# Kernel optimization log

Measured on AMD Instinct MI355X. Metric: run time of the kernel, lower is better.

## Reference

```python
import jax, jax.numpy as jnp
import numpy as np

NEG_SLOPE = 0.2  # PyG GATConv default negative_slope
BN_EPS = 1e-5


def gat_layer(x, src, dst, W, b, a_src, a_dst, heads, out_ch, concat):
    # x: [N, Fin]; W: [Fin, heads*out_ch]; a_src/a_dst: [heads, out_ch]
    N = x.shape[0]
    h = (x @ W).reshape(N, heads, out_ch)
    s = (h * a_src).sum(-1)            # [N, H]
    d = (h * a_dst).sum(-1)            # [N, H]
    e = jax.nn.leaky_relu(s[src] + d[dst], NEG_SLOPE)   # [E, H]
    # segment softmax over incoming edges of each destination node
    m = jax.ops.segment_max(e, dst, num_segments=N)
    ex = jnp.exp(e - m[dst])
    denom = jax.ops.segment_sum(ex, dst, num_segments=N)
    alpha = ex / (denom[dst] + 1e-16)                   # [E, H]
    out = jax.ops.segment_sum(alpha[:, :, None] * h[src], dst, num_segments=N)  # [N,H,C]
    out = out.reshape(N, heads * out_ch) if concat else out.mean(axis=1)
    return out + b


def batchnorm(x, gamma, beta):
    mu = x.mean(axis=0)
    var = x.var(axis=0)
    return gamma * (x - mu) * jax.lax.rsqrt(var + BN_EPS) + beta


def setup_inputs() -> dict:
    key = jax.random.key(0)
    ks = jax.random.split(key, 24)
    N, E, Fin, Hd, heads, C = 50000, 800000, 128, 64, 4, 2
    wdim = Hd * heads  # 256
    inp = {
        'x': jax.random.normal(ks[0], (N, Fin), jnp.float32),
        'edge_index': jax.random.randint(ks[1], (2, E), 0, N, jnp.int64),
    }
    def glorot(k, shape):
        fan = shape[0] + shape[-1]
        return jax.random.normal(k, shape, jnp.float32) * np.sqrt(2.0 / fan)
    # layer 0: Fin -> heads x Hd (concat)
    inp['W0'] = glorot(ks[2], (Fin, wdim)); inp['b0'] = jnp.zeros((wdim,), jnp.float32)
    inp['asrc0'] = glorot(ks[3], (heads, Hd)); inp['adst0'] = glorot(ks[4], (heads, Hd))
    inp['g0'] = jnp.ones((wdim,), jnp.float32); inp['be0'] = jnp.zeros((wdim,), jnp.float32)
    # layer 1: wdim -> heads x Hd (concat)
    inp['W1'] = glorot(ks[5], (wdim, wdim)); inp['b1'] = jnp.zeros((wdim,), jnp.float32)
    inp['asrc1'] = glorot(ks[6], (heads, Hd)); inp['adst1'] = glorot(ks[7], (heads, Hd))
    inp['g1'] = jnp.ones((wdim,), jnp.float32); inp['be1'] = jnp.zeros((wdim,), jnp.float32)
    # layer 2: wdim -> 1 head x Hd (no concat)
    inp['W2'] = glorot(ks[8], (wdim, Hd)); inp['b2'] = jnp.zeros((Hd,), jnp.float32)
    inp['asrc2'] = glorot(ks[9], (1, Hd)); inp['adst2'] = glorot(ks[10], (1, Hd))
    inp['g2'] = jnp.ones((Hd,), jnp.float32); inp['be2'] = jnp.zeros((Hd,), jnp.float32)
    # classifier: Linear(2*Hd, Hd) -> ReLU -> Linear(Hd, C)
    inp['Wc1'] = glorot(ks[11], (2 * Hd, Hd)); inp['bc1'] = jnp.zeros((Hd,), jnp.float32)
    inp['Wc2'] = glorot(ks[12], (Hd, C)); inp['bc2'] = jnp.zeros((C,), jnp.float32)
    return inp


def reference(x, edge_index, W0, b0, asrc0, adst0, g0, be0,
              W1, b1, asrc1, adst1, g1, be1,
              W2, b2, asrc2, adst2, g2, be2,
              Wc1, bc1, Wc2, bc2):
    N = x.shape[0]
    # add self-loops (PyG GATConv default)
    loops = jnp.arange(N, dtype=edge_index.dtype)
    src = jnp.concatenate([edge_index[0], loops])
    dst = jnp.concatenate([edge_index[1], loops])
    heads, Hd = asrc0.shape[0], asrc0.shape[1]

    h = gat_layer(x, src, dst, W0, b0, asrc0, adst0, heads, Hd, True)
    h = jax.nn.relu(batchnorm(h, g0, be0))
    h = gat_layer(h, src, dst, W1, b1, asrc1, adst1, heads, Hd, True)
    h = jax.nn.relu(batchnorm(h, g1, be1))
    h = gat_layer(h, src, dst, W2, b2, asrc2, adst2, 1, Hd, False)
    h = jax.nn.relu(batchnorm(h, g2, be2))

    pooled = jnp.concatenate([h.mean(axis=0, keepdims=True),
                              h.max(axis=0, keepdims=True)], axis=1)  # [1, 2*Hd]
    z = jax.nn.relu(pooled @ Wc1 + bc1)
    return z @ Wc2 + bc2  # [1, num_classes]
```

## Files before the change

kernel.cpp:

```cpp
#include <hip/hip_runtime.h>


typedef unsigned int uint;
typedef unsigned short ushort;

#define NEG_SLOPE 0.2f
#define BN_EPS 1e-5f
#define NB_RED 256

__device__ __forceinline__ float bf2f(uint u) { return __uint_as_float(u << 16); }
__device__ __forceinline__ ushort f2bf(float f) {
    uint u = __float_as_uint(f);
    u += 0x7fff + ((u >> 16) & 1);
    return (ushort)(u >> 16);
}
__device__ __forceinline__ float lrelu(float x) { return x > 0.f ? x : NEG_SLOPE * x; }


__global__ void hist_kernel(const int* __restrict__ ei, int* __restrict__ deg, int E) {
    int e = blockIdx.x * blockDim.x + threadIdx.x;
    if (e < E) atomicAdd(&deg[ei[E + e]], 1);
}

__global__ void scan_part(const int* __restrict__ deg, int* __restrict__ offsets,
                          int* __restrict__ bsum, int N) {
    __shared__ int sh[256];
    int t = threadIdx.x;
    int base = blockIdx.x * 1024 + t * 4;
    int v0 = (base + 0 < N) ? deg[base + 0] : 0;
    int v1 = (base + 1 < N) ? deg[base + 1] : 0;
    int v2 = (base + 2 < N) ? deg[base + 2] : 0;
    int v3 = (base + 3 < N) ? deg[base + 3] : 0;
    int s = v0 + v1 + v2 + v3;
    sh[t] = s;
    __syncthreads();
    for (int off = 1; off < 256; off <<= 1) {
        int y = (t >= off) ? sh[t - off] : 0;
        __syncthreads();
        sh[t] += y;
        __syncthreads();
    }
    int p = sh[t] - s;
    if (base + 0 < N) offsets[base + 0] = p;
    p += v0;
    if (base + 1 < N) offsets[base + 1] = p;
    p += v1;
    if (base + 2 < N) offsets[base + 2] = p;
    p += v2;
    if (base + 3 < N) offsets[base + 3] = p;
    if (t == 255) bsum[blockIdx.x] = sh[255];
}

__global__ void scan_top(const int* __restrict__ bsum, int* __restrict__ bexcl,
                         int nb, int* __restrict__ offsets, int N) {
    if (threadIdx.x == 0) {
        int run = 0;
        for (int b = 0; b < nb; ++b) { bexcl[b] = run; run += bsum[b]; }
        offsets[N] = run;
    }
}

__global__ void scan_add(int* __restrict__ offsets, int* __restrict__ cursor,
                         const int* __restrict__ bexcl, int N) {
    int add = bexcl[blockIdx.x];
    int base = blockIdx.x * 1024 + threadIdx.x * 4;
#pragma unroll
    for (int k = 0; k < 4; ++k) {
        int i = base + k;
        if (i < N) { int v = offsets[i] + add; offsets[i] = v; cursor[i] = v; }
    }
}

__global__ void scatter_kernel(const int* __restrict__ ei, int* __restrict__ cursor,
                               int* __restrict__ srcs, int E) {
    int e = blockIdx.x * blockDim.x + threadIdx.x;
    if (e < E) {
        int s = ei[e];
        int d = ei[E + e];
        int p = atomicAdd(&cursor[d], 1);
        srcs[p] = s;
    }
}


__global__ void cvt_x_kernel(const float* __restrict__ x, ushort* __restrict__ xb,
                             int total_real, int total_pad) {
    int i = blockIdx.x * blockDim.x + threadIdx.x;
    if (i < total_pad) xb[i] = (i < total_real) ? f2bf(x[i]) : (ushort)0;
}

__global__ void transpose_all_kernel(const float* __restrict__ W0, ushort* __restrict__ w0t,
                                     const float* __restrict__ W1, ushort* __restrict__ w1t,
                                     const float* __restrict__ W2, ushort* __restrict__ w2t) {
    int i = blockIdx.x * blockDim.x + threadIdx.x;
    if (i < 32768) {
        int n = i / 128, k = i - n * 128;
        w0t[i] = f2bf(W0[(size_t)k * 256 + n]);
    } else if (i < 32768 + 65536) {
        int j = i - 32768;
        int n = j / 256, k = j - n * 256;
        w1t[j] = f2bf(W1[(size_t)k * 256 + n]);
    } else if (i < 32768 + 65536 + 16384) {
        int j = i - 32768 - 65536;
        int n = j / 256, k = j - n * 256;
        w2t[j] = f2bf(W2[(size_t)k * 64 + n]);
    }
}


typedef __attribute__((ext_vector_type(8))) short bf16x8;
typedef __attribute__((ext_vector_type(4))) float floatx4;

template <int BN, int H>
__launch_bounds__(256)
__global__ void mfma_gemm_bt(const ushort* __restrict__ A, const ushort* __restrict__ Bt,
                             ushort* __restrict__ C, const float* __restrict__ asrc,
                             const float* __restrict__ adst, float* __restrict__ sv,
                             float* __restrict__ dv, int K, int Nn) {
    constexpr int WCOLS = (BN == 128) ? 2 : 1;
    constexpr int WROWS = 4 / WCOLS;
    constexpr int MT = 128 / (WROWS * 16);
    constexpr int NT = BN / (WCOLS * 16);
    constexpr int BCALLS = (BN * 32 * 2) / 4096;

    __shared__ ushort As[128 * 32];
    __shared__ ushort Bs[BN * 32];

    int t = threadIdx.x;
    int w = t >> 6, l = t & 63;
    int row0 = blockIdx.x * 128;
    int col0 = blockIdx.y * BN;
    int wr = (w / WCOLS) * (MT * 16);
    int wc = (w % WCOLS) * (NT * 16);

    floatx4 acc[MT][NT];
#pragma unroll
    for (int mi = 0; mi < MT; ++mi)
#pragma unroll
        for (int ni = 0; ni < NT; ++ni)
#pragma unroll
            for (int r = 0; r < 4; ++r) acc[mi][ni][r] = 0.f;

    int mrow = l & 15;
    int kc = (l >> 4) * 8;

    for (int kt = 0; kt < K; kt += 32) {
#pragma unroll
        for (int c = 0; c < 2; ++c) {
            int idx = c * 256 + t;
            const ushort* gp = A + (size_t)(row0 + (idx >> 2)) * K + kt + (idx & 3) * 8;
            __builtin_amdgcn_global_load_lds(
                (const __attribute__((address_space(1))) void*)gp,
                (__attribute__((address_space(3))) void*)(As + (idx & ~63) * 8),
                16, 0, 0);
        }
#pragma unroll
        for (int c = 0; c < BCALLS; ++c) {
            int idx = c * 256 + t;
            const ushort* gp = Bt + (size_t)(col0 + (idx >> 2)) * K + kt + (idx & 3) * 8;
            __builtin_amdgcn_global_load_lds(
                (const __attribute__((address_space(1))) void*)gp,
                (__attribute__((address_space(3))) void*)(Bs + (idx & ~63) * 8),
                16, 0, 0);
        }
        __syncthreads();

        bf16x8 af[MT], bfr[NT];
#pragma unroll
        for (int mi = 0; mi < MT; ++mi)
            af[mi] = *(const bf16x8*)&As[(wr + mi * 16 + mrow) * 32 + kc];
#pragma unroll
        for (int ni = 0; ni < NT; ++ni)
            bfr[ni] = *(const bf16x8*)&Bs[(wc + ni * 16 + mrow) * 32 + kc];
#pragma unroll
        for (int mi = 0; mi < MT; ++mi)
#pragma unroll
            for (int ni = 0; ni < NT; ++ni)
                acc[mi][ni] = __builtin_amdgcn_mfma_f32_16x16x32_bf16(
                    af[mi], bfr[ni], acc[mi][ni], 0, 0, 0);
        __syncthreads();
    }

#pragma unroll
    for (int mi = 0; mi < MT; ++mi) {
        int rbase = row0 + wr + mi * 16 + (l >> 4) * 4;
#pragma unroll
        for (int ni = 0; ni < NT; ++ni) {
            int col = col0 + wc + ni * 16 + (l & 15);
#pragma unroll
            for (int r = 0; r < 4; ++r)
                C[(size_t)(rbase + r) * Nn + col] = f2bf(acc[mi][ni][r]);
        }
    }

    float av[NT], bv[NT];
#pragma unroll
    for (int ni = 0; ni < NT; ++ni) {
        int ch = col0 + wc + ni * 16 + (l & 15);
        av[ni] = asrc[ch];
        bv[ni] = adst[ch];
    }
    int gh = (col0 + wc) >> 6;
#pragma unroll
    for (int mi = 0; mi < MT; ++mi) {
#pragma unroll
        for (int r = 0; r < 4; ++r) {
            float s = 0.f, d = 0.f;
#pragma unroll
            for (int ni = 0; ni < NT; ++ni) {
                float hv = acc[mi][ni][r];
                s += hv * av[ni];
                d += hv * bv[ni];
            }
#pragma unroll
            for (int m = 8; m >= 1; m >>= 1) {
                s += __shfl_xor(s, m);
                d += __shfl_xor(d, m);
            }
            if ((l & 15) == 0) {
                int row = row0 + wr + mi * 16 + (l >> 4) * 4 + r;
                sv[row * H + gh] = s;
                dv[row * H + gh] = d;
            }
        }
    }
}


__launch_bounds__(128)
__global__ void agg4_kernel(const ushort* __restrict__ hb, const float* __restrict__ sv,
                            const float* __restrict__ dv, const int* __restrict__ offsets,
                            const int* __restrict__ srcs, const float* __restrict__ bias,
                            ushort* __restrict__ zb, int N) {
    int i = blockIdx.x;
    int t = threadIdx.x, g = t >> 5;
    int beg = offsets[i], end = offsets[i + 1];

    float d_i = dv[i * 4 + g];
    float wself = __expf(fminf(lrelu(sv[i * 4 + g] + d_i), 60.f));

    uint p = *(const uint*)&hb[(size_t)i * 256 + 2 * t];
    float ax = wself * bf2f(p & 0xffffu);
    float ay = wself * bf2f(p >> 16);
    float den = wself;

    int j = beg;
    int srcn_next = (j < end) ? srcs[j] : 0;
    for (; j < end;) {
        int srcn = srcn_next;
        float sval = sv[srcn * 4 + g];
        uint q = *(const uint*)&hb[(size_t)srcn * 256 + 2 * t];
        ++j;
        if (j < end) srcn_next = srcs[j];
        float wgt = __expf(fminf(lrelu(sval + d_i), 60.f));
        ax += wgt * bf2f(q & 0xffffu);
        ay += wgt * bf2f(q >> 16);
        den += wgt;
    }
    float rden = 1.f / (den + 1e-16f);
    ax = ax * rden + bias[2 * t];
    ay = ay * rden + bias[2 * t + 1];
    *(uint*)&zb[(size_t)i * 256 + 2 * t] = (uint)f2bf(ax) | ((uint)f2bf(ay) << 16);
}

__launch_bounds__(64)
__global__ void agg1_kernel(const ushort* __restrict__ hb, const float* __restrict__ sv,
                            const float* __restrict__ dv, const int* __restrict__ offsets,
                            const int* __restrict__ srcs, const float* __restrict__ bias,
                            ushort* __restrict__ zb, int N) {
    int i = blockIdx.x;
    int lane = threadIdx.x;
    int beg = offsets[i], end = offsets[i + 1];

    float d_i = dv[i];
    float wself = __expf(fminf(lrelu(sv[i] + d_i), 60.f));
    float acc = wself * bf2f(hb[(size_t)i * 64 + lane]);
    float den = wself;

    int j = beg;
    int srcn_next = (j < end) ? srcs[j] : 0;
    for (; j < end;) {
        int srcn = srcn_next;
        float sval = sv[srcn];
        float hv = bf2f(hb[(size_t)srcn * 64 + lane]);
        ++j;
        if (j < end) srcn_next = srcs[j];
        float wgt = __expf(fminf(lrelu(sval + d_i), 60.f));
        acc += wgt * hv;
        den += wgt;
    }
    zb[(size_t)i * 64 + lane] = f2bf(acc / (den + 1e-16f) + bias[lane]);
}


template <int F>
__launch_bounds__(256)
__global__ void bn_stats_kernel(const ushort* __restrict__ x, float* __restrict__ ps,
                                float* __restrict__ pq, int N) {
    constexpr int OCT = F / 8;
    __shared__ float lds_s[F], lds_q[F];
    int t = threadIdx.x;
    if (t < F) { lds_s[t] = 0.f; lds_q[t] = 0.f; }
    __syncthreads();

    float s[8] = {}, q[8] = {};
    int total8 = N * F / 8;
    for (int idx = blockIdx.x * 256 + t; idx < total8; idx += NB_RED * 256) {
        uint4 v = ((const uint4*)x)[idx];
        uint pr[4] = {v.x, v.y, v.z, v.w};
#pragma unroll
        for (int k = 0; k < 4; ++k) {
            float a = bf2f(pr[k] & 0xffffu);
            float b = bf2f(pr[k] >> 16);
            s[2 * k] += a;     q[2 * k] += a * a;
            s[2 * k + 1] += b; q[2 * k + 1] += b * b;
        }
    }
    int co = t % OCT;
#pragma unroll
    for (int j = 0; j < 8; ++j) {
        atomicAdd(&lds_s[co * 8 + j], s[j]);
        atomicAdd(&lds_q[co * 8 + j], q[j]);
    }
    __syncthreads();
    if (t < F) {
        ps[blockIdx.x * F + t] = lds_s[t];
        pq[blockIdx.x * F + t] = lds_q[t];
    }
}

__global__ void bn_final_kernel(const float* __restrict__ ps, const float* __restrict__ pq,
                                const float* __restrict__ g, const float* __restrict__ be,
                                float* __restrict__ scale, float* __restrict__ shift,
                                int N, int F) {
    int t = threadIdx.x;
    if (t < F) {
        float s = 0.f, q = 0.f;
        for (int b = 0; b < NB_RED; ++b) { s += ps[b * F + t]; q += pq[b * F + t]; }
        float mean = s / (float)N;
        float var = q / (float)N - mean * mean;
        float sc = g[t] * rsqrtf(var + BN_EPS);
        scale[t] = sc;
        shift[t] = be[t] - sc * mean;
    }
}

__global__ void bn_apply_kernel(uint* __restrict__ x, const float* __restrict__ scale,
                                const float* __restrict__ shift, int totalPairs, int Fmask) {
    int i = blockIdx.x * blockDim.x + threadIdx.x;
    if (i < totalPairs) {
        uint p = x[i];
        int c0 = (2 * i) & Fmask;
        float v0 = fmaxf(bf2f(p & 0xffffu) * scale[c0] + shift[c0], 0.f);
        float v1 = fmaxf(bf2f(p >> 16) * scale[c0 + 1] + shift[c0 + 1], 0.f);
        x[i] = (uint)f2bf(v0) | ((uint)f2bf(v1) << 16);
    }
}


__launch_bounds__(256)
__global__ void pool_kernel(const ushort* __restrict__ y, const float* __restrict__ scale,
                            const float* __restrict__ shift, float* __restrict__ psum,
                            float* __restrict__ pmax, int N) {
    constexpr int F = 64, OCT = 8;
    __shared__ float lds_s[F];
    __shared__ uint lds_m[F];
    int t = threadIdx.x;
    if (t < F) { lds_s[t] = 0.f; lds_m[t] = 0u; }
    __syncthreads();

    int co = t % OCT;
    float sc[8], sh[8];
#pragma unroll
    for (int j = 0; j < 8; ++j) { sc[j] = scale[co * 8 + j]; sh[j] = shift[co * 8 + j]; }

    float s[8] = {}, m[8] = {};
    int total8 = N * F / 8;
    for (int idx = blockIdx.x * 256 + t; idx < total8; idx += NB_RED * 256) {
        uint4 v = ((const uint4*)y)[idx];
        uint pr[4] = {v.x, v.y, v.z, v.w};
#pragma unroll
        for (int k = 0; k < 4; ++k) {
            float a = fmaxf(bf2f(pr[k] & 0xffffu) * sc[2 * k] + sh[2 * k], 0.f);
            float b = fmaxf(bf2f(pr[k] >> 16) * sc[2 * k + 1] + sh[2 * k + 1], 0.f);
            s[2 * k] += a;     m[2 * k] = fmaxf(m[2 * k], a);
            s[2 * k + 1] += b; m[2 * k + 1] = fmaxf(m[2 * k + 1], b);
        }
    }
#pragma unroll
    for (int j = 0; j < 8; ++j) {
        atomicAdd(&lds_s[co * 8 + j], s[j]);
        atomicMax(&lds_m[co * 8 + j], __float_as_uint(m[j]));
    }
    __syncthreads();
    if (t < F) {
        psum[blockIdx.x * F + t] = lds_s[t];
        pmax[blockIdx.x * F + t] = __uint_as_float(lds_m[t]);
    }
}

__global__ void classify_kernel(const float* __restrict__ psum, const float* __restrict__ pmax,
                                const float* __restrict__ Wc1, const float* __restrict__ bc1,
                                const float* __restrict__ Wc2, const float* __restrict__ bc2,
                                float* __restrict__ out, int N) {
    __shared__ float pooled[128];
    __shared__ float z[64];
    int t = threadIdx.x;
    if (t < 64) {
        float s = 0.f;
        for (int b = 0; b < NB_RED; ++b) s += psum[b * 64 + t];
        pooled[t] = s / (float)N;
    } else {
        int c = t - 64;
        float m = 0.f;
        for (int b = 0; b < NB_RED; ++b) m = fmaxf(m, pmax[b * 64 + c]);
        pooled[t] = m;
    }
    __syncthreads();
    if (t < 64) {
        float a = bc1[t];
        for (int k = 0; k < 128; ++k) a += pooled[k] * Wc1[k * 64 + t];
        z[t] = a > 0.f ? a : 0.f;
    }
    __syncthreads();
    if (t < 2) {
        float a = bc2[t];
        for (int j = 0; j < 64; ++j) a += z[j] * Wc2[j * 2 + t];
        out[t] = a;
    }
}


extern "C" void kernel_launch(void* const* d_in, const int* in_sizes, int n_in,
                              void* d_out, int out_size, void* d_ws, size_t ws_size,
                              hipStream_t stream) {
    const float* x   = (const float*)d_in[0];
    const int*   ei  = (const int*)d_in[1];
    const float* W0  = (const float*)d_in[2];  const float* b0  = (const float*)d_in[3];
    const float* as0 = (const float*)d_in[4];  const float* ad0 = (const float*)d_in[5];
    const float* g0  = (const float*)d_in[6];  const float* be0 = (const float*)d_in[7];
    const float* W1  = (const float*)d_in[8];  const float* b1  = (const float*)d_in[9];
    const float* as1 = (const float*)d_in[10]; const float* ad1 = (const float*)d_in[11];
    const float* g1  = (const float*)d_in[12]; const float* be1 = (const float*)d_in[13];
    const float* W2  = (const float*)d_in[14]; const float* b2  = (const float*)d_in[15];
    const float* as2 = (const float*)d_in[16]; const float* ad2 = (const float*)d_in[17];
    const float* g2  = (const float*)d_in[18]; const float* be2 = (const float*)d_in[19];
    const float* Wc1 = (const float*)d_in[20]; const float* bc1 = (const float*)d_in[21];
    const float* Wc2 = (const float*)d_in[22]; const float* bc2 = (const float*)d_in[23];
    float* out = (float*)d_out;

    const int N = in_sizes[0] / 128;
    const int E = in_sizes[1] / 2;
    const int Mpad = ((N + 127) / 128) * 128;
    const int NB_SCAN = (N + 1023) / 1024;

    char* ws = (char*)d_ws;
    size_t o = 0;
    auto alloc = [&](size_t bytes) -> void* {
        void* p = ws + o;
        o = (o + bytes + 255) & ~(size_t)255;
        return p;
    };
    int*    deg     = (int*)alloc((size_t)N * 4);
    int*    offsets = (int*)alloc((size_t)(N + 1) * 4);
    int*    cursor  = (int*)alloc((size_t)N * 4);
    int*    srcs    = (int*)alloc((size_t)E * 4);
    int*    bsum    = (int*)alloc((size_t)NB_SCAN * 4);
    int*    bexcl   = (int*)alloc((size_t)NB_SCAN * 4);
    ushort* xb      = (ushort*)alloc((size_t)Mpad * 128 * 2);
    ushort* w0t     = (ushort*)alloc((size_t)256 * 128 * 2);
    ushort* w1t     = (ushort*)alloc((size_t)256 * 256 * 2);
    ushort* w2t     = (ushort*)alloc((size_t)64 * 256 * 2);
    ushort* hb      = (ushort*)alloc((size_t)Mpad * 256 * 2);
    ushort* zb      = (ushort*)alloc((size_t)Mpad * 256 * 2);
    float*  sv      = (float*)alloc((size_t)Mpad * 4 * 4);
    float*  dv      = (float*)alloc((size_t)Mpad * 4 * 4);
    float*  ps      = (float*)alloc((size_t)NB_RED * 256 * 4);
    float*  pq      = (float*)alloc((size_t)NB_RED * 256 * 4);
    float*  scale   = (float*)alloc(256 * 4);
    float*  shift   = (float*)alloc(256 * 4);
    float*  psum    = (float*)alloc((size_t)NB_RED * 64 * 4);
    float*  pmax    = (float*)alloc((size_t)NB_RED * 64 * 4);

    hipMemsetAsync(deg, 0, (size_t)N * 4, stream);
    int eb = (E + 255) / 256;
    hist_kernel<<<eb, 256, 0, stream>>>(ei, deg, E);
    scan_part<<<NB_SCAN, 256, 0, stream>>>(deg, offsets, bsum, N);
    scan_top<<<1, 64, 0, stream>>>(bsum, bexcl, NB_SCAN, offsets, N);
    scan_add<<<NB_SCAN, 256, 0, stream>>>(offsets, cursor, bexcl, N);
    scatter_kernel<<<eb, 256, 0, stream>>>(ei, cursor, srcs, E);

    cvt_x_kernel<<<(Mpad * 128 + 255) / 256, 256, 0, stream>>>(x, xb, N * 128, Mpad * 128);
    transpose_all_kernel<<<(32768 + 65536 + 16384 + 255) / 256, 256, 0, stream>>>(
        W0, w0t, W1, w1t, W2, w2t);

    {
        dim3 gg(Mpad / 128, 2);
        mfma_gemm_bt<128, 4><<<gg, 256, 0, stream>>>(xb, w0t, hb, as0, ad0, sv, dv, 128, 256);
        agg4_kernel<<<N, 128, 0, stream>>>(hb, sv, dv, offsets, srcs, b0, zb, N);
        bn_stats_kernel<256><<<NB_RED, 256, 0, stream>>>(zb, ps, pq, N);
        bn_final_kernel<<<1, 256, 0, stream>>>(ps, pq, g0, be0, scale, shift, N, 256);
        bn_apply_kernel<<<(N * 128 + 255) / 256, 256, 0, stream>>>((uint*)zb, scale, shift,
                                                                   N * 128, 255);
    }
    {
        dim3 gg(Mpad / 128, 2);
        mfma_gemm_bt<128, 4><<<gg, 256, 0, stream>>>(zb, w1t, hb, as1, ad1, sv, dv, 256, 256);
        agg4_kernel<<<N, 128, 0, stream>>>(hb, sv, dv, offsets, srcs, b1, zb, N);
        bn_stats_kernel<256><<<NB_RED, 256, 0, stream>>>(zb, ps, pq, N);
        bn_final_kernel<<<1, 256, 0, stream>>>(ps, pq, g1, be1, scale, shift, N, 256);
        bn_apply_kernel<<<(N * 128 + 255) / 256, 256, 0, stream>>>((uint*)zb, scale, shift,
                                                                   N * 128, 255);
    }
    {
        dim3 gg(Mpad / 128, 1);
        mfma_gemm_bt<64, 1><<<gg, 256, 0, stream>>>(zb, w2t, hb, as2, ad2, sv, dv, 256, 64);
        agg1_kernel<<<N, 64, 0, stream>>>(hb, sv, dv, offsets, srcs, b2, zb, N);
        bn_stats_kernel<64><<<NB_RED, 256, 0, stream>>>(zb, ps, pq, N);
        bn_final_kernel<<<1, 64, 0, stream>>>(ps, pq, g2, be2, scale, shift, N, 64);
    }

    pool_kernel<<<NB_RED, 256, 0, stream>>>(zb, scale, shift, psum, pmax, N);
    classify_kernel<<<1, 128, 0, stream>>>(psum, pmax, Wc1, bc1, Wc2, bc2, out, N);
}
```

Before: 686.6 us.

## Split neighbor aggregation across edge groups with vector loads, fuse prep kernels

The aggregation kernels now process four incoming edges in parallel, one per thread group. Each thread loads a wider vector of features (16 bytes per lane in agg4, 8 bytes in agg1), and the partial sums are reduced through LDS or shuffles before the self-loop term and normalization are applied. This aims to expose more memory-level parallelism in the latency-bound gather over irregular neighbor lists. Separately, the x conversion, weight transposes and degree histogram are merged into one launch to cut launch overhead. In exchange, agg4 adds an LDS reduction and a barrier, and the summation order changes.

```diff
diff --git a/kernel.cpp b/kernel.cpp
--- a/kernel.cpp
+++ b/kernel.cpp
@@ -17,10 +17,39 @@
 __device__ __forceinline__ float lrelu(float x) { return x > 0.f ? x : NEG_SLOPE * x; }
 
 
-__global__ void hist_kernel(const int* __restrict__ ei, int* __restrict__ deg, int E) {
-    int e = blockIdx.x * blockDim.x + threadIdx.x;
-    if (e < E) atomicAdd(&deg[ei[E + e]], 1);
-}
+__global__ void prep_kernel(const float* __restrict__ x, ushort* __restrict__ xb,
+                            int total_real, int total_pad,
+                            const float* __restrict__ W0, ushort* __restrict__ w0t,
+                            const float* __restrict__ W1, ushort* __restrict__ w1t,
+                            const float* __restrict__ W2, ushort* __restrict__ w2t,
+                            const int* __restrict__ ei, int* __restrict__ deg, int E) {
+    int i = blockIdx.x * blockDim.x + threadIdx.x;
+    if (i < total_pad) {
+        xb[i] = (i < total_real) ? f2bf(x[i]) : (ushort)0;
+        return;
+    }
+    int j = i - total_pad;
+    if (j < 32768) {
+        int n = j / 128, k = j - n * 128;
+        w0t[j] = f2bf(W0[(size_t)k * 256 + n]);
+        return;
+    }
+    j -= 32768;
+    if (j < 65536) {
+        int n = j / 256, k = j - n * 256;
+        w1t[j] = f2bf(W1[(size_t)k * 256 + n]);
+        return;
+    }
+    j -= 65536;
+    if (j < 16384) {
+        int n = j / 256, k = j - n * 256;
+        w2t[j] = f2bf(W2[(size_t)k * 64 + n]);
+        return;
+    }
+    j -= 16384;
+    if (j < E) atomicAdd(&deg[ei[E + j]], 1);
+}
+
 
 __global__ void scan_part(const int* __restrict__ deg, int* __restrict__ offsets,
                           int* __restrict__ bsum, int N) {
@@ -79,31 +108,6 @@
         int d = ei[E + e];
         int p = atomicAdd(&cursor[d], 1);
         srcs[p] = s;
-    }
-}
-
-
-__global__ void cvt_x_kernel(const float* __restrict__ x, ushort* __restrict__ xb,
-                             int total_real, int total_pad) {
-    int i = blockIdx.x * blockDim.x + threadIdx.x;
-    if (i < total_pad) xb[i] = (i < total_real) ? f2bf(x[i]) : (ushort)0;
-}
-
-__global__ void transpose_all_kernel(const float* __restrict__ W0, ushort* __restrict__ w0t,
-                                     const float* __restrict__ W1, ushort* __restrict__ w1t,
-                                     const float* __restrict__ W2, ushort* __restrict__ w2t) {
-    int i = blockIdx.x * blockDim.x + threadIdx.x;
-    if (i < 32768) {
-        int n = i / 128, k = i - n * 128;
-        w0t[i] = f2bf(W0[(size_t)k * 256 + n]);
-    } else if (i < 32768 + 65536) {
-        int j = i - 32768;
-        int n = j / 256, k = j - n * 256;
-        w1t[j] = f2bf(W1[(size_t)k * 256 + n]);
-    } else if (i < 32768 + 65536 + 16384) {
-        int j = i - 32768 - 65536;
-        int n = j / 256, k = j - n * 256;
-        w2t[j] = f2bf(W2[(size_t)k * 64 + n]);
     }
 }
 
@@ -232,36 +236,56 @@
                             const float* __restrict__ dv, const int* __restrict__ offsets,
                             const int* __restrict__ srcs, const float* __restrict__ bias,
                             ushort* __restrict__ zb, int N) {
+    __shared__ float lsum[4][256];
+    __shared__ float lden[4][4];
+
     int i = blockIdx.x;
-    int t = threadIdx.x, g = t >> 5;
+    int t = threadIdx.x;
+    int grp = t >> 5, gl = t & 31;
+    int head = gl >> 3;
     int beg = offsets[i], end = offsets[i + 1];
 
-    float d_i = dv[i * 4 + g];
-    float wself = __expf(fminf(lrelu(sv[i * 4 + g] + d_i), 60.f));
-
+    float d_i = dv[i * 4 + head];
+    float ax[8] = {};
+    float den = 0.f;
+
+    int j = beg + grp;
+    int srcn = (j < end) ? srcs[j] : 0;
+    while (j < end) {
+        float sval = sv[srcn * 4 + head];
+        uint4 q = *(const uint4*)&hb[(size_t)srcn * 256 + gl * 8];
+        int jn = j + 4;
+        int srcn_n = (jn < end) ? srcs[jn] : 0;
+        float wgt = __expf(fminf(lrelu(sval + d_i), 60.f));
+        den += wgt;
+        uint pr[4] = {q.x, q.y, q.z, q.w};
+#pragma unroll
+        for (int k = 0; k < 4; ++k) {
+            ax[2 * k]     += wgt * bf2f(pr[k] & 0xffffu);
+            ax[2 * k + 1] += wgt * bf2f(pr[k] >> 16);
+        }
+        j = jn; srcn = srcn_n;
+    }
+
+#pragma unroll
+    for (int k = 0; k < 8; ++k) lsum[grp][gl * 8 + k] = ax[k];
+    if ((gl & 7) == 0) lden[grp][head] = den;
+    __syncthreads();
+
+    int h = t >> 5;
+    float wself = __expf(fminf(lrelu(sv[i * 4 + h] + dv[i * 4 + h]), 60.f));
+    float dtot = lden[0][h] + lden[1][h] + lden[2][h] + lden[3][h] + wself + 1e-16f;
+    float rden = 1.f / dtot;
     uint p = *(const uint*)&hb[(size_t)i * 256 + 2 * t];
-    float ax = wself * bf2f(p & 0xffffu);
-    float ay = wself * bf2f(p >> 16);
-    float den = wself;
-
-    int j = beg;
-    int srcn_next = (j < end) ? srcs[j] : 0;
-    for (; j < end;) {
-        int srcn = srcn_next;
-        float sval = sv[srcn * 4 + g];
-        uint q = *(const uint*)&hb[(size_t)srcn * 256 + 2 * t];
-        ++j;
-        if (j < end) srcn_next = srcs[j];
-        float wgt = __expf(fminf(lrelu(sval + d_i), 60.f));
-        ax += wgt * bf2f(q & 0xffffu);
-        ay += wgt * bf2f(q >> 16);
-        den += wgt;
-    }
-    float rden = 1.f / (den + 1e-16f);
-    ax = ax * rden + bias[2 * t];
-    ay = ay * rden + bias[2 * t + 1];
-    *(uint*)&zb[(size_t)i * 256 + 2 * t] = (uint)f2bf(ax) | ((uint)f2bf(ay) << 16);
-}
+    float a0 = lsum[0][2 * t] + lsum[1][2 * t] + lsum[2][2 * t] + lsum[3][2 * t]
+             + wself * bf2f(p & 0xffffu);
+    float a1 = lsum[0][2 * t + 1] + lsum[1][2 * t + 1] + lsum[2][2 * t + 1]
+             + lsum[3][2 * t + 1] + wself * bf2f(p >> 16);
+    a0 = a0 * rden + bias[2 * t];
+    a1 = a1 * rden + bias[2 * t + 1];
+    *(uint*)&zb[(size_t)i * 256 + 2 * t] = (uint)f2bf(a0) | ((uint)f2bf(a1) << 16);
+}
+
 
 __launch_bounds__(64)
 __global__ void agg1_kernel(const ushort* __restrict__ hb, const float* __restrict__ sv,
@@ -269,27 +293,51 @@
                             const int* __restrict__ srcs, const float* __restrict__ bias,
                             ushort* __restrict__ zb, int N) {
     int i = blockIdx.x;
-    int lane = threadIdx.x;
+    int l = threadIdx.x;
+    int grp = l >> 4, gl = l & 15;
     int beg = offsets[i], end = offsets[i + 1];
 
     float d_i = dv[i];
-    float wself = __expf(fminf(lrelu(sv[i] + d_i), 60.f));
-    float acc = wself * bf2f(hb[(size_t)i * 64 + lane]);
-    float den = wself;
-
-    int j = beg;
-    int srcn_next = (j < end) ? srcs[j] : 0;
-    for (; j < end;) {
-        int srcn = srcn_next;
+    float ax[4] = {};
+    float den = 0.f;
+
+    int j = beg + grp;
+    int srcn = (j < end) ? srcs[j] : 0;
+    while (j < end) {
         float sval = sv[srcn];
-        float hv = bf2f(hb[(size_t)srcn * 64 + lane]);
-        ++j;
-        if (j < end) srcn_next = srcs[j];
+        uint2 q = *(const uint2*)&hb[(size_t)srcn * 64 + gl * 4];
+        int jn = j + 4;
+        int srcn_n = (jn < end) ? srcs[jn] : 0;
         float wgt = __expf(fminf(lrelu(sval + d_i), 60.f));
-        acc += wgt * hv;
         den += wgt;
-    }
-    zb[(size_t)i * 64 + lane] = f2bf(acc / (den + 1e-16f) + bias[lane]);
+        ax[0] += wgt * bf2f(q.x & 0xffffu);
+        ax[1] += wgt * bf2f(q.x >> 16);
+        ax[2] += wgt * bf2f(q.y & 0xffffu);
+        ax[3] += wgt * bf2f(q.y >> 16);
+        j = jn; srcn = srcn_n;
+    }
+
+#pragma unroll
+    for (int k = 0; k < 4; ++k) {
+        ax[k] += __shfl_xor(ax[k], 16);
+        ax[k] += __shfl_xor(ax[k], 32);
+    }
+    den += __shfl_xor(den, 16);
+    den += __shfl_xor(den, 32);
+
+    if (l < 16) {
+        float wself = __expf(fminf(lrelu(sv[i] + d_i), 60.f));
+        float rden = 1.f / (den + wself + 1e-16f);
+        uint2 q = *(const uint2*)&hb[(size_t)i * 64 + gl * 4];
+        float a0 = (ax[0] + wself * bf2f(q.x & 0xffffu)) * rden + bias[gl * 4 + 0];
+        float a1 = (ax[1] + wself * bf2f(q.x >> 16)) * rden + bias[gl * 4 + 1];
+        float a2 = (ax[2] + wself * bf2f(q.y & 0xffffu)) * rden + bias[gl * 4 + 2];
+        float a3 = (ax[3] + wself * bf2f(q.y >> 16)) * rden + bias[gl * 4 + 3];
+        uint2 o;
+        o.x = (uint)f2bf(a0) | ((uint)f2bf(a1) << 16);
+        o.y = (uint)f2bf(a2) | ((uint)f2bf(a3) << 16);
+        *(uint2*)&zb[(size_t)i * 64 + gl * 4] = o;
+    }
 }
 
 
@@ -483,16 +531,14 @@
     float*  pmax    = (float*)alloc((size_t)NB_RED * 64 * 4);
 
     hipMemsetAsync(deg, 0, (size_t)N * 4, stream);
-    int eb = (E + 255) / 256;
-    hist_kernel<<<eb, 256, 0, stream>>>(ei, deg, E);
+    int prep_total = Mpad * 128 + 32768 + 65536 + 16384 + E;
+    prep_kernel<<<(prep_total + 255) / 256, 256, 0, stream>>>(
+        x, xb, N * 128, Mpad * 128, W0, w0t, W1, w1t, W2, w2t, ei, deg, E);
+
     scan_part<<<NB_SCAN, 256, 0, stream>>>(deg, offsets, bsum, N);
     scan_top<<<1, 64, 0, stream>>>(bsum, bexcl, NB_SCAN, offsets, N);
     scan_add<<<NB_SCAN, 256, 0, stream>>>(offsets, cursor, bexcl, N);
-    scatter_kernel<<<eb, 256, 0, stream>>>(ei, cursor, srcs, E);
-
-    cvt_x_kernel<<<(Mpad * 128 + 255) / 256, 256, 0, stream>>>(x, xb, N * 128, Mpad * 128);
-    transpose_all_kernel<<<(32768 + 65536 + 16384 + 255) / 256, 256, 0, stream>>>(
-        W0, w0t, W1, w1t, W2, w2t);
+    scatter_kernel<<<(E + 255) / 256, 256, 0, stream>>>(ei, cursor, srcs, E);
 
     {
         dim3 gg(Mpad / 128, 2);
```

New measurement: 584.2 us. 1.18x faster.
